# Optimization experiments

Hardware: AMD Instinct MI355X
Metric: run time of the kernel (lower is better)

Reference implementation:

```python
import jax, jax.numpy as jnp
import numpy as np

ANGLE_THR = float(np.pi / 2.0)
N_PTS = 3072
# nuScenes per-class anchor sizes (l, w, h) hard-coded in FrustumClusterProposer.__init__
ANCHORS = np.array([[4.63, 1.97, 1.74], [6.93, 2.51, 2.84], [6.37, 2.85, 3.19],
                    [10.5, 2.94, 3.47], [12.29, 2.9, 3.87], [0.5, 2.53, 0.98],
                    [2.11, 0.77, 1.47], [1.7, 0.6, 1.28], [0.73, 0.67, 1.77],
                    [0.41, 0.41, 1.07]], dtype=np.float32)


def setup_inputs() -> dict:
    key = jax.random.key(0)
    k1, k2 = jax.random.split(key)
    pts = jax.random.normal(k1, (N_PTS, 3), jnp.float32) * 15.0  # metric-scale frustum points
    lbl = jax.random.randint(k2, (N_PTS,), 0, 10)                # per-point 2D-detector class id
    return {"frust_points": pts, "frust_labels": lbl, "anchors": jnp.asarray(ANCHORS)}


def _cluster(points, labels_cls, anchors, angle_thr=ANGLE_THR):
    """Faithful port of CombinedAngleClusterer.__call__ (greedy angle/dist clustering + merge)."""
    n = points.shape[0]
    f32 = points.dtype
    pos = jnp.arange(n)

    # curr_anchor_max_diffs: xy replaced by max(l, w) per class
    xy_max = anchors[:, :2].max(axis=1)
    amd = jnp.stack([xy_max, xy_max, anchors[:, 2]], axis=1)  # [10, 3]
    anchor_r2 = jnp.linalg.norm(anchors, axis=1) / 2.0        # [10]

    # pairwise displacements, distances and calc_angles matrix (vectorized over rows)
    diff = points[None, :, :] - points[:, None, :]            # [n, n, 3]
    dists = jnp.linalg.norm(diff, axis=-1)                    # cdist
    dot = -jnp.einsum('id,ijd->ij', points, diff)             # l1 = -p_i, l2 = p_j - p_i
    denom = jnp.linalg.norm(points, axis=1)[:, None] * dists + 1e-8
    angles = jnp.arccos(jnp.clip(dot / denom, -1.0, 1.0))     # clip for numerical safety

    dl0 = jnp.full((n,), -1, jnp.int32).at[0].set(0)          # dist_labels
    cc0 = jnp.full((n,), -1, jnp.int32)                       # cluster_classes

    def step(carry, _):
        dl, cc, cur, lab = carry
        cls_cur = labels_cls[cur]
        cc = cc.at[lab].set(jnp.where(cc[lab] < 0, cls_cur, cc[lab]))
        nv = dl == -1                                          # not visited
        cm = dl == lab                                         # current cluster
        cmf = cm.astype(f32)
        centre = (points * cmf[:, None]).sum(0) / cmf.sum()
        drow = dists[cur]
        dmin = jnp.min(jnp.where(nv, drow, jnp.inf))
        dmax = jnp.max(jnp.where(nv, drow, -jnp.inf))
        dcost = (drow - dmin) / (dmax - dmin + 1e-8)           # norm01 over unvisited
        lcost = jnp.minimum(jnp.abs(labels_cls - cls_cur).astype(f32), 1.0)
        ci = jnp.argmin(jnp.where(nv, dcost + lcost, jnp.inf))
        d = points[cur] - points[ci]
        new_c = (jnp.any(jnp.abs(d) > amd[cls_cur])
                 | (jnp.max(jnp.where(cm, angles[cur], -jnp.inf)) < angle_thr)
                 | (labels_cls[ci] != cls_cur)
                 | (jnp.linalg.norm(d) > anchor_r2[cls_cur])
                 | (jnp.linalg.norm(centre - points[ci]) > anchor_r2[cls_cur]))
        lab = lab + new_c.astype(jnp.int32)
        dl = dl.at[ci].set(lab)
        return (dl, cc, ci, lab), None

    (dl, cc, _, _), _ = jax.lax.scan(step, (dl0, cc0, jnp.int32(0), jnp.int32(0)), None, length=n - 1)

    # cluster statistics (padded to n clusters; num_clusters = max label, EXCLUSIVE, as in torch)
    counts = jax.ops.segment_sum(jnp.ones((n,), jnp.int32), dl, num_segments=n)
    centres = jax.ops.segment_sum(points, dl, num_segments=n) / jnp.maximum(counts, 1).astype(f32)[:, None]
    num_clusters = dl.max()
    order = jnp.argsort(-jnp.where(pos < num_clusters, counts, -1))
    ocls = cc[order]
    ocentres = centres[order]

    def merge(carry, i):
        keep, dl = carry
        idx = order[i]
        active = (i < num_clusters) & keep[i]
        r2 = anchor_r2[cc[idx]]
        cond = (active & (pos > i) & (pos < num_clusters) & keep
                & (ocls == cc[idx])
                & (jnp.linalg.norm(ocentres - centres[idx], axis=1) < r2))
        keep = keep & ~cond
        merged = jnp.zeros((n,), bool).at[order].set(cond)     # order-position -> cluster-id
        dl = jnp.where(merged[dl], idx, dl)
        return (keep, dl), None

    (_, dl), _ = jax.lax.scan(merge, (jnp.ones((n,), bool), dl), pos)
    return dl


def reference(frust_points, frust_labels, anchors):
    return _cluster(frust_points, frust_labels.astype(jnp.int32), anchors)
```

## Files before the change

kernel.cpp:

```cpp
#include <hip/hip_runtime.h>
#include <math.h>

#define NPTS 3072
#define BLK  256
#define NW   4
#define NSL  8
#define NKB  48
#define NCLS 10

#pragma clang fp contract(off)

__device__ __forceinline__ unsigned umin32(unsigned a, unsigned b) { return a < b ? a : b; }

__device__ __forceinline__ unsigned rowmin4_u32(unsigned x) {
    unsigned t;
    t = (unsigned)__builtin_amdgcn_update_dpp(-1, (int)x, 0x111, 0xF, 0xF, false); x = x < t ? x : t;
    t = (unsigned)__builtin_amdgcn_update_dpp(-1, (int)x, 0x112, 0xF, 0xF, false); x = x < t ? x : t;
    t = (unsigned)__builtin_amdgcn_update_dpp(-1, (int)x, 0x114, 0xF, 0xF, false); x = x < t ? x : t;
    t = (unsigned)__builtin_amdgcn_update_dpp(-1, (int)x, 0x118, 0xF, 0xF, false); x = x < t ? x : t;
    return x;
}

__device__ __forceinline__ unsigned wavemin_u32(unsigned x) {
    unsigned r = rowmin4_u32(x);
    unsigned a = (unsigned)__builtin_amdgcn_readlane((int)r, 15);
    unsigned b = (unsigned)__builtin_amdgcn_readlane((int)r, 31);
    unsigned c = (unsigned)__builtin_amdgcn_readlane((int)r, 47);
    unsigned d = (unsigned)__builtin_amdgcn_readlane((int)r, 63);
    return umin32(umin32(a, b), umin32(c, d));
}

__device__ __forceinline__ float readlanef(float v, int l) {
    return __int_as_float(__builtin_amdgcn_readlane(__float_as_int(v), l));
}

template<int NS>
__device__ __forceinline__ void sweep_step(const float (&sxr)[NSL], const float (&syr)[NSL],
                                           const float (&szr)[NSL], const unsigned (&mmr)[NSL],
                                           float pcx, float pcy, float pcz,
                                           unsigned &kbest, unsigned &mbest,
                                           float &bx, float &by, float &bz)
{
    float ss[NS];
    #pragma unroll
    for (int i = 0; i < NS; ++i) {
        float dx = pcx - sxr[i], dy = pcy - syr[i], dz = pcz - szr[i];
        ss[i] = (dx*dx + dy*dy) + dz*dz;
    }
    float m;
    if constexpr (NS == 5)
        m = fminf(fminf(fminf(ss[0], ss[1]), fminf(ss[2], ss[3])), ss[4]);
    else if constexpr (NS == 6)
        m = fminf(fminf(fminf(ss[0], ss[1]), fminf(ss[2], ss[3])), fminf(ss[4], ss[5]));
    else
        m = fminf(fminf(fminf(ss[0], ss[1]), fminf(ss[2], ss[3])),
                  fminf(fminf(ss[4], ss[5]), fminf(ss[6], ss[7])));
    kbest = __float_as_uint(m);
    unsigned mb = 0xFFFFFFFFu;
    #pragma unroll
    for (int i = 0; i < NS; ++i) {
        unsigned ci = (ss[i] == m) ? mmr[i] : 0xFFFFFFFFu;
        mb = umin32(mb, ci);
    }
    mbest = mb;
    bx = sxr[0]; by = syr[0]; bz = szr[0];
    #pragma unroll
    for (int i = 1; i < NS; ++i) {
        bool w = (mmr[i] == mb);
        bx = w ? sxr[i] : bx; by = w ? syr[i] : by; bz = w ? szr[i] : bz;
    }
}

template<int NS>
__device__ __forceinline__ void poison_step(float (&sxr)[NSL], const unsigned (&mmr)[NSL],
                                            unsigned wm)
{
    #pragma unroll
    for (int i = 0; i < NS; ++i)
        if (mmr[i] == wm) sxr[i] = 3e19f;
}

#define WALK_INNER(NS)                                                          \
    _Pragma("unroll 4")                                                         \
    for (int k = 0; k < iters; ++k) {                                           \
        float icx = sx / scnt, icy = sy / scnt, icz = sz / scnt;                \
        unsigned kbest, mbest; float bx, by, bz;                                \
        sweep_step<NS>(sxr, syr, szr, mmr, pcx, pcy, pcz, kbest, mbest, bx, by, bz); \
        unsigned wk = wavemin_u32(kbest);                                       \
        bool cand = (kbest == wk);                                              \
        unsigned long long msk = __ballot(cand);                                \
        if (msk & (msk - 1)) {                     \
            unsigned wm2 = wavemin_u32(cand ? mbest : 0xFFFFFFFFu);             \
            msk = __ballot(cand && (mbest == wm2));                             \
        }                                                                       \
        int wl = __ffsll((unsigned long long)msk) - 1;                          \
        unsigned wm = (unsigned)__builtin_amdgcn_readlane((int)mbest, wl);      \
        float pix = readlanef(bx, wl), piy = readlanef(by, wl), piz = readlanef(bz, wl); \
        pos = (int)(wm & 0xFFFu);                                               \
        poison_step<NS>(sxr, mmr, wm);                                          \
        float dx = pcx - pix, dy = pcy - piy, dz = pcz - piz;                   \
        bool a1 = (fabsf(dx) > amdxy_c) | (fabsf(dy) > amdxy_c) | (fabsf(dz) > amdz_c); \
        float ex = icx - pix, ey = icy - piy, ez = icz - piz;                   \
        float seC = (ex*ex + ey*ey) + ez*ez;                                    \
        bool nc = a1 | (wk > Vc) | (__float_as_uint(seC) > Vc);                 \
        lab += (int)nc;                                                         \
        su = nc ? u : su;                                                       \
        *((lane == 0) ? &startv[lab] : &sdump[lane]) = (unsigned short)su;      \
        scnt = nc ? 1.0f : (scnt + 1.0f);                                       \
        sx = nc ? pix : (sx + pix);                                             \
        sy = nc ? piy : (sy + piy);                                             \
        sz = nc ? piz : (sz + piz);                                             \
        capv = (lane == (u & 63)) ? (unsigned)pos : capv;                       \
        vor16[(u & ~63) + lane] = (unsigned short)capv;                         \
        pcx = pix; pcy = piy; pcz = piz;                                        \
        ++u;                                                                    \
    }

__global__ __launch_bounds__(BLK)
void frustum_cluster(const float* __restrict__ pts,
                     const int* __restrict__ lblg,
                     const float* __restrict__ anch,
                     int* __restrict__ out,
                     int* __restrict__ ws)
{
    const int tid  = threadIdx.x;
    const int lane = tid & 63;
    const int wid  = tid >> 6;

    int*    dlg    = ws + 16;
    float4* gstats = (float4*)(ws + 8192);

    __shared__ float4 gpts[NPTS];
    __shared__ unsigned short vor16[NPTS];
    __shared__ unsigned short startv[NPTS];
    __shared__ unsigned short sdump[64];
    __shared__ float amdxy[NCLS], amdz[NCLS];
    __shared__ unsigned vthr[NCLS], wthr[NCLS];
    __shared__ int cntL[NCLS], curL[NCLS], baseL[NCLS];
    __shared__ int cntC[NCLS], curC[NCLS], baseC[NCLS];
    __shared__ int p0s, nclusS;

    if (tid < NCLS) {
        float l = anch[tid*3+0], w = anch[tid*3+1], h = anch[tid*3+2];
        amdxy[tid] = fmaxf(l, w);
        amdz[tid]  = h;
        float r2 = sqrtf((l*l + w*w) + h*h) * 0.5f;
        unsigned lo = 0u, hi = 0x7F7FFFFFu;
        while (hi - lo > 1u) {
            unsigned mid = lo + ((hi - lo) >> 1);
            if (sqrtf(__uint_as_float(mid)) <= r2) lo = mid; else hi = mid;
        }
        vthr[tid] = lo;
        lo = 0u; hi = 0x7F7FFFFFu;
        while (hi - lo > 1u) {
            unsigned mid = lo + ((hi - lo) >> 1);
            if (sqrtf(__uint_as_float(mid)) < r2) lo = mid; else hi = mid;
        }
        wthr[tid] = lo;
        cntL[tid] = 0; curL[tid] = 0; cntC[tid] = 0; curC[tid] = 0;
    }
    __syncthreads();
    for (int j = tid; j < NPTS; j += BLK) atomicAdd(&cntL[lblg[j]], 1);
    __syncthreads();
    if (tid == 0) { int acc = 0; for (int c = 0; c < NCLS; ++c) { baseL[c] = acc; acc += cntL[c]; } }
    __syncthreads();
    for (int j = tid; j < NPTS; j += BLK) {
        int c = lblg[j];
        int pos = baseL[c] + atomicAdd(&curL[c], 1);
        float4 e;
        e.x = pts[3*j]; e.y = pts[3*j+1]; e.z = pts[3*j+2];
        e.w = __uint_as_float(((unsigned)j << 16) | ((unsigned)c << 12) | (unsigned)pos);
        gpts[pos] = e;
        if (j == 0) p0s = pos;
    }
    if (tid == 0) startv[0] = 0;
    __syncthreads();

    if (wid == 0) {
        float axyL = 0.f, azL = 0.f; int vLn = 0, baseLn = 0, cntLn = 0;
        if (lane < NCLS) {
            axyL = amdxy[lane]; azL = amdz[lane];
            vLn = (int)vthr[lane]; baseLn = baseL[lane]; cntLn = cntL[lane];
        }
        const int p0 = p0s;
        int pos = p0;
        int cls = lblg[0];
        unsigned walked = 1u << cls;
        float sxr[NSL], syr[NSL], szr[NSL];
        unsigned mmr[NSL];
        float pcx = pts[0], pcy = pts[1], pcz = pts[2];
        float sx = pcx, sy = pcy, sz = pcz, scnt = 1.0f;
        int lab = 0;
        int su  = 0;
        unsigned capv = (unsigned)p0;
        int u = 1;

        for (int wix = 0; wix < NCLS; ++wix) {
            int base_c = __builtin_amdgcn_readlane(baseLn, cls);
            int cnt_c  = __builtin_amdgcn_readlane(cntLn, cls);
            #pragma unroll
            for (int i = 0; i < NSL; ++i) {
                int off = lane + (i << 6);
                int p = base_c + off;
                bool in = off < cnt_c;
                float4 e = gpts[in ? p : 0];
                bool v = in && (p != pos);
                sxr[i] = v ? e.x : 3e19f;
                syr[i] = v ? e.y : 0.f;
                szr[i] = v ? e.z : 0.f;
                mmr[i] = in ? __float_as_uint(e.w) : 0xFFFFFFFFu;
            }
            float amdxy_c = readlanef(axyL, cls), amdz_c = readlanef(azL, cls);
            unsigned Vc = (unsigned)__builtin_amdgcn_readlane(vLn, cls);
            int nsC = (cnt_c + 63) >> 6;
            int iters = cnt_c - 1;

            if (nsC <= 5)      { WALK_INNER(5) }
            else if (nsC == 6) { WALK_INNER(6) }
            else               { WALK_INNER(8) }

            if (u >= NPTS) break;

            {
                unsigned kbest = 0xFFFFFFFFu, mbest = 0xFFFFFFFFu;
                float bx = 0.f, by = 0.f, bz = 0.f;
                for (int k2 = 0; k2 < NKB; ++k2) {
                    int p = lane + (k2 << 6);
                    float4 e = gpts[p];
                    unsigned meta = __float_as_uint(e.w);
                    float dx = pcx - e.x, dy = pcy - e.y, dz = pcz - e.z;
                    float s = (dx*dx + dy*dy) + dz*dz;
                    unsigned key = __float_as_uint(s);
                    bool ok = !((walked >> ((meta >> 12) & 15u)) & 1u);
                    if (ok && (key < kbest || (key == kbest && meta < mbest))) {
                        kbest = key; mbest = meta; bx = e.x; by = e.y; bz = e.z;
                    }
                }
                unsigned wk = wavemin_u32(kbest);
                bool cand = (kbest == wk);
                unsigned wm = wavemin_u32(cand ? mbest : 0xFFFFFFFFu);
                unsigned long long msk = __ballot(cand && (mbest == wm));
                int wl = __ffsll((unsigned long long)msk) - 1;
                float pix = readlanef(bx, wl), piy = readlanef(by, wl), piz = readlanef(bz, wl);
                pos = (int)(wm & 0xFFFu);
                cls = (int)((wm >> 12) & 15u);
                walked |= 1u << cls;
                lab += 1;
                su = u;
                if (lane == 0) startv[lab] = (unsigned short)u;
                sx = pix; sy = piy; sz = piz; scnt = 1.0f;
                capv = (lane == (u & 63)) ? (unsigned)pos : capv;
                vor16[(u & ~63) + lane] = (unsigned short)capv;
                pcx = pix; pcy = piy; pcz = piz;
                ++u;
            }
        }
        if (lane == 0) nclusS = lab;
    }
    __syncthreads();
    const int nclus = nclusS;

    for (int c2 = tid; c2 <= nclus; c2 += BLK) {
        int s0 = startv[c2];
        int s1e = (c2 < nclus) ? (int)startv[c2+1] : NPTS;
        float ax = 0.f, ay = 0.f, az = 0.f;
        int clsF = 0;
        for (int s = s0; s < s1e; ++s) {
            float4 e = gpts[vor16[s]];
            unsigned pk = __float_as_uint(e.w);
            if (s == s0) clsF = (int)((pk >> 12) & 15u);
            ax = ax + e.x; ay = ay + e.y; az = az + e.z;
            dlg[pk >> 16] = c2;
        }
        if (c2 < nclus) {
            float fc = (float)(s1e - s0);
            float4 g;
            g.x = ax / fc; g.y = ay / fc; g.z = az / fc;
            g.w = __uint_as_float(((unsigned)(s1e - s0) << 4) | (unsigned)clsF);
            gstats[c2] = g;
        }
    }
    __syncthreads();

    for (int c2 = tid; c2 < nclus; c2 += BLK)
        atomicAdd(&cntC[__float_as_uint(gstats[c2].w) & 15u], 1);
    __syncthreads();
    if (tid == 0) { int acc = 0; for (int c = 0; c < NCLS; ++c) { baseC[c] = acc; acc += cntC[c]; } }
    __syncthreads();

    for (int c2 = tid; c2 < nclus; c2 += BLK) {
        unsigned gw = __float_as_uint(gstats[c2].w);
        int cl = (int)(gw & 15u);
        int slot = baseC[cl] + atomicAdd(&curC[cl], 1);
        vor16[slot]  = (unsigned short)(gw >> 4);
        startv[slot] = (unsigned short)c2;
    }
    __syncthreads();

    for (int slot = tid; slot < nclus; slot += BLK) {
        int cl = 0;
        #pragma unroll
        for (int q = 1; q < NCLS; ++q) cl += (int)(slot >= baseC[q]);
        int b0 = baseC[cl], b1 = b0 + cntC[cl];
        int cnt = (int)vor16[slot], id = (int)startv[slot];
        int r = 0;
        for (int s2 = b0; s2 < b1; ++s2) {
            int cnt2 = (int)vor16[s2], id2 = (int)startv[s2];
            r += (int)((cnt2 > cnt) || (cnt2 == cnt && id2 < id));
        }
        float4 g = gstats[id];
        float4 oe;
        oe.x = g.x; oe.y = g.y; oe.z = g.z;
        oe.w = __uint_as_float(((unsigned)id << 1) | 1u);
        gpts[b0 + r] = oe;
    }
    __syncthreads();

    unsigned short* remap16 = startv;
    for (int c2 = tid; c2 < NPTS; c2 += BLK) remap16[c2] = (unsigned short)c2;
    __syncthreads();

    for (int cl = wid; cl < NCLS; cl += NW) {
        int b0 = baseC[cl], b1 = b0 + cntC[cl];
        unsigned Wc = wthr[cl];
        for (int i = b0; i < b1; ++i) {
            float4 ei = gpts[i];
            unsigned wi = __float_as_uint(ei.w);
            if (wi & 1u) {
                int orgI = (int)(wi >> 1);
                for (int j = i + 1 + lane; j < b1; j += 64) {
                    float4 ej = gpts[j];
                    unsigned wj = __float_as_uint(ej.w);
                    if (wj & 1u) {
                        float ddx = ej.x - ei.x, ddy = ej.y - ei.y, ddz = ej.z - ei.z;
                        float sdd = (ddx*ddx + ddy*ddy) + ddz*ddz;
                        if (__float_as_uint(sdd) <= Wc) {
                            gpts[j].w = __uint_as_float(wj & ~1u);
                            remap16[wj >> 1] = (unsigned short)orgI;
                        }
                    }
                }
            }
        }
    }
    __syncthreads();

    for (int p = tid; p < NPTS; p += BLK) out[p] = (int)remap16[dlg[p]];
}

extern "C" void kernel_launch(void* const* d_in, const int* in_sizes, int n_in,
                              void* d_out, int out_size, void* d_ws, size_t ws_size,
                              hipStream_t stream) {
    const float* pts  = (const float*)d_in[0];
    const int*   lbl  = (const int*)d_in[1];
    const float* anch = (const float*)d_in[2];
    frustum_cluster<<<dim3(1), dim3(BLK), 0, stream>>>(pts, lbl, anch,
                                                       (int*)d_out, (int*)d_ws);
}
```

Measured before the change: 2.255 ms.

## Split cluster-boundary decisions out of the serial walk into a parallel per-walk pass

The serial greedy walk now only records the visit order of points and the start and class of each per-class walk. Deciding where a new cluster begins (anchor box test, distance threshold, running-centroid test) and keeping the running sums move to a later pass in which each lane replays one walk in parallel. A compaction step then gathers the per-walk cluster start lists. This shortens the loop-carried critical path of the single-wave walk, at the cost of an extra replay pass, extra barriers and more shared-memory bookkeeping.

```diff
diff --git a/kernel.cpp b/kernel.cpp
--- a/kernel.cpp
+++ b/kernel.cpp
@@ -83,7 +83,6 @@
 #define WALK_INNER(NS)                                                          \
     _Pragma("unroll 4")                                                         \
     for (int k = 0; k < iters; ++k) {                                           \
-        float icx = sx / scnt, icy = sy / scnt, icz = sz / scnt;                \
         unsigned kbest, mbest; float bx, by, bz;                                \
         sweep_step<NS>(sxr, syr, szr, mmr, pcx, pcy, pcz, kbest, mbest, bx, by, bz); \
         unsigned wk = wavemin_u32(kbest);                                       \
@@ -98,20 +97,7 @@
         float pix = readlanef(bx, wl), piy = readlanef(by, wl), piz = readlanef(bz, wl); \
         pos = (int)(wm & 0xFFFu);                                               \
         poison_step<NS>(sxr, mmr, wm);                                          \
-        float dx = pcx - pix, dy = pcy - piy, dz = pcz - piz;                   \
-        bool a1 = (fabsf(dx) > amdxy_c) | (fabsf(dy) > amdxy_c) | (fabsf(dz) > amdz_c); \
-        float ex = icx - pix, ey = icy - piy, ez = icz - piz;                   \
-        float seC = (ex*ex + ey*ey) + ez*ez;                                    \
-        bool nc = a1 | (wk > Vc) | (__float_as_uint(seC) > Vc);                 \
-        lab += (int)nc;                                                         \
-        su = nc ? u : su;                                                       \
-        *((lane == 0) ? &startv[lab] : &sdump[lane]) = (unsigned short)su;      \
-        scnt = nc ? 1.0f : (scnt + 1.0f);                                       \
-        sx = nc ? pix : (sx + pix);                                             \
-        sy = nc ? piy : (sy + piy);                                             \
-        sz = nc ? piz : (sz + piz);                                             \
-        capv = (lane == (u & 63)) ? (unsigned)pos : capv;                       \
-        vor16[(u & ~63) + lane] = (unsigned short)capv;                         \
+        *((lane == 0) ? &recM16[u] : &sdump[lane]) = (unsigned short)pos;       \
         pcx = pix; pcy = piy; pcz = piz;                                        \
         ++u;                                                                    \
     }
@@ -131,13 +117,16 @@
     float4* gstats = (float4*)(ws + 8192);
 
     __shared__ float4 gpts[NPTS];
-    __shared__ unsigned short vor16[NPTS];
+    __shared__ unsigned short recM16[NPTS];
     __shared__ unsigned short startv[NPTS];
     __shared__ unsigned short sdump[64];
+    __shared__ unsigned short walkS16[65];
+    __shared__ unsigned short walkCls16[16];
     __shared__ float amdxy[NCLS], amdz[NCLS];
     __shared__ unsigned vthr[NCLS], wthr[NCLS];
     __shared__ int cntL[NCLS], curL[NCLS], baseL[NCLS];
     __shared__ int cntC[NCLS], curC[NCLS], baseC[NCLS];
+    __shared__ int cntW[16], baseW[16];
     __shared__ int p0s, nclusS;
 
     if (tid < NCLS) {
@@ -159,6 +148,8 @@
         wthr[tid] = lo;
         cntL[tid] = 0; curL[tid] = 0; cntC[tid] = 0; curC[tid] = 0;
     }
+    if (tid < 65) walkS16[tid] = (unsigned short)NPTS;
+    if (tid < 16) { walkCls16[tid] = 0; cntW[tid] = 0; }
     __syncthreads();
     for (int j = tid; j < NPTS; j += BLK) atomicAdd(&cntL[lblg[j]], 1);
     __syncthreads();
@@ -173,15 +164,11 @@
         gpts[pos] = e;
         if (j == 0) p0s = pos;
     }
-    if (tid == 0) startv[0] = 0;
     __syncthreads();
 
     if (wid == 0) {
-        float axyL = 0.f, azL = 0.f; int vLn = 0, baseLn = 0, cntLn = 0;
-        if (lane < NCLS) {
-            axyL = amdxy[lane]; azL = amdz[lane];
-            vLn = (int)vthr[lane]; baseLn = baseL[lane]; cntLn = cntL[lane];
-        }
+        int baseLn = 0, cntLn = 0;
+        if (lane < NCLS) { baseLn = baseL[lane]; cntLn = cntL[lane]; }
         const int p0 = p0s;
         int pos = p0;
         int cls = lblg[0];
@@ -189,13 +176,14 @@
         float sxr[NSL], syr[NSL], szr[NSL];
         unsigned mmr[NSL];
         float pcx = pts[0], pcy = pts[1], pcz = pts[2];
-        float sx = pcx, sy = pcy, sz = pcz, scnt = 1.0f;
-        int lab = 0;
-        int su  = 0;
-        unsigned capv = (unsigned)p0;
         int u = 1;
+        if (lane == 0) recM16[0] = (unsigned short)p0;
 
         for (int wix = 0; wix < NCLS; ++wix) {
+            if (lane == 0) {
+                walkS16[wix]   = (unsigned short)(u - 1);
+                walkCls16[wix] = (unsigned short)cls;
+            }
             int base_c = __builtin_amdgcn_readlane(baseLn, cls);
             int cnt_c  = __builtin_amdgcn_readlane(cntLn, cls);
             #pragma unroll
@@ -210,8 +198,6 @@
                 szr[i] = v ? e.z : 0.f;
                 mmr[i] = in ? __float_as_uint(e.w) : 0xFFFFFFFFu;
             }
-            float amdxy_c = readlanef(axyL, cls), amdz_c = readlanef(azL, cls);
-            unsigned Vc = (unsigned)__builtin_amdgcn_readlane(vLn, cls);
             int nsC = (cnt_c + 63) >> 6;
             int iters = cnt_c - 1;
 
@@ -245,17 +231,76 @@
                 pos = (int)(wm & 0xFFFu);
                 cls = (int)((wm >> 12) & 15u);
                 walked |= 1u << cls;
-                lab += 1;
-                su = u;
-                if (lane == 0) startv[lab] = (unsigned short)u;
-                sx = pix; sy = piy; sz = piz; scnt = 1.0f;
-                capv = (lane == (u & 63)) ? (unsigned)pos : capv;
-                vor16[(u & ~63) + lane] = (unsigned short)capv;
+                *((lane == 0) ? &recM16[u] : &sdump[lane]) = (unsigned short)pos;
                 pcx = pix; pcy = piy; pcz = piz;
                 ++u;
             }
         }
-        if (lane == 0) nclusS = lab;
+    }
+    __syncthreads();
+
+    if (wid == 0) {
+        int w = lane;
+        int sW = (int)walkS16[w];
+        int eW = (int)walkS16[w + 1];
+        bool exists = sW < NPTS;
+        int cls = (int)walkCls16[exists ? w : 0];
+        float axy = amdxy[cls], az = amdz[cls];
+        unsigned Vc = vthr[cls];
+        int pos0 = (int)recM16[exists ? sW : 0];
+        float4 pe = gpts[pos0];
+        float prevx = pe.x, prevy = pe.y, prevz = pe.z;
+        float sx = prevx, sy = prevy, sz = prevz, scnt = 1.0f;
+        int cnt = 1;
+        if (exists) startv[sW] = (unsigned short)sW;
+        int u = sW + 1;
+        int posn = (int)recM16[(exists && u < eW) ? u : 0];
+        for (;;) {
+            unsigned long long alive = __ballot(u < eW);
+            if (!alive) break;
+            bool act = (u < eW);
+            float4 ec = gpts[act ? posn : 0];
+            int posn2 = (int)recM16[(u + 1 < eW) ? (u + 1) : 0];
+            float pix = ec.x, piy = ec.y, piz = ec.z;
+            float dx = prevx - pix, dy = prevy - piy, dz = prevz - piz;
+            float seS = (dx*dx + dy*dy) + dz*dz;
+            bool a1 = (fabsf(dx) > axy) | (fabsf(dy) > axy) | (fabsf(dz) > az);
+            float icx = sx / scnt, icy = sy / scnt, icz = sz / scnt;
+            float ex = icx - pix, ey = icy - piy, ez = icz - piz;
+            float seC = (ex*ex + ey*ey) + ez*ez;
+            bool nc = a1 | (__float_as_uint(seS) > Vc) | (__float_as_uint(seC) > Vc);
+            if (act & nc) startv[sW + cnt] = (unsigned short)u;
+            cnt += (act & nc) ? 1 : 0;
+            scnt = nc ? 1.0f : (scnt + 1.0f);
+            sx = nc ? pix : (sx + pix);
+            sy = nc ? piy : (sy + piy);
+            sz = nc ? piz : (sz + piz);
+            prevx = pix; prevy = piy; prevz = piz;
+            posn = posn2;
+            ++u;
+        }
+        if (exists) cntW[w] = cnt;
+    }
+    __syncthreads();
+
+    if (tid == 0) {
+        int acc = 0;
+        for (int c = 0; c < NCLS; ++c) { baseW[c] = acc; acc += cntW[c]; }
+        nclusS = acc - 1;
+    }
+    __syncthreads();
+
+    if (wid == 0) {
+        for (int w2 = 0; w2 < NCLS; ++w2) {
+            int sW = (int)walkS16[w2];
+            if (sW >= NPTS) break;
+            int bW = baseW[w2], cW = cntW[w2];
+            if (bW == sW) continue;
+            for (int j = lane; j < cW; j += 64) {
+                unsigned short v = startv[sW + j];
+                startv[bW + j] = v;
+            }
+        }
     }
     __syncthreads();
     const int nclus = nclusS;
@@ -266,7 +311,7 @@
         float ax = 0.f, ay = 0.f, az = 0.f;
         int clsF = 0;
         for (int s = s0; s < s1e; ++s) {
-            float4 e = gpts[vor16[s]];
+            float4 e = gpts[recM16[s]];
             unsigned pk = __float_as_uint(e.w);
             if (s == s0) clsF = (int)((pk >> 12) & 15u);
             ax = ax + e.x; ay = ay + e.y; az = az + e.z;
@@ -292,7 +337,7 @@
         unsigned gw = __float_as_uint(gstats[c2].w);
         int cl = (int)(gw & 15u);
         int slot = baseC[cl] + atomicAdd(&curC[cl], 1);
-        vor16[slot]  = (unsigned short)(gw >> 4);
+        recM16[slot] = (unsigned short)(gw >> 4);
         startv[slot] = (unsigned short)c2;
     }
     __syncthreads();
@@ -302,10 +347,10 @@
         #pragma unroll
         for (int q = 1; q < NCLS; ++q) cl += (int)(slot >= baseC[q]);
         int b0 = baseC[cl], b1 = b0 + cntC[cl];
-        int cnt = (int)vor16[slot], id = (int)startv[slot];
+        int cnt = (int)recM16[slot], id = (int)startv[slot];
         int r = 0;
         for (int s2 = b0; s2 < b1; ++s2) {
-            int cnt2 = (int)vor16[s2], id2 = (int)startv[s2];
+            int cnt2 = (int)recM16[s2], id2 = (int)startv[s2];
             r += (int)((cnt2 > cnt) || (cnt2 == cnt && id2 < id));
         }
         float4 g = gstats[id];
```

Result: faster. 1.808 ms, median of 2 (-19.8%).
